# Optimization experiments

Hardware: AMD Instinct MI355X
Metric: run time of the kernel (lower is better)

Reference implementation:

```python
import jax, jax.numpy as jnp
import numpy as np

NEG_SLOPE = 0.2  # PyG GATConv default negative_slope


def _glorot(key, shape):
    fan = shape[0]
    return jax.random.normal(key, shape, dtype=jnp.float32) / np.sqrt(fan)


def setup_inputs() -> dict:
    key = jax.random.key(0)
    ks = jax.random.split(key, 32)
    N, E, C_IN, C_H, C_OUT = 20000, 320000, 128, 640, 2
    inp = {
        "x": jax.random.normal(ks[0], (N, C_IN), dtype=jnp.float32),
        "edge_index": jax.random.randint(ks[1], (2, E), 0, N, dtype=jnp.int64),
    }
    dims = [(C_IN, C_H), (C_H, C_H), (C_H, C_H), (C_H, C_H), (C_H, C_OUT)]
    for i, (ci, co) in enumerate(dims, start=1):
        k = jax.random.split(ks[1 + i], 4)
        inp[f"W{i}"] = _glorot(k[0], (ci, co))
        inp[f"as{i}"] = _glorot(k[1], (co,))
        inp[f"ad{i}"] = _glorot(k[2], (co,))
        inp[f"b{i}"] = jnp.zeros((co,), dtype=jnp.float32)
    return inp


def _gat_conv(h, W, a_src, a_dst, b, src, dst, N):
    # h: [N, Ci] -> hW: [N, Co]
    hW = h @ W
    # per-edge attention logit: LeakyReLU(alpha_src[j] + alpha_dst[i]) for edge j->i
    e = jax.nn.leaky_relu((hW @ a_src)[src] + (hW @ a_dst)[dst], NEG_SLOPE)
    # segment softmax over incoming edges of each dst node (self-loops guarantee nonempty)
    m = jax.ops.segment_max(e, dst, num_segments=N)
    ex = jnp.exp(e - m[dst])
    den = jax.ops.segment_sum(ex, dst, num_segments=N)
    alpha = ex / den[dst]
    # weighted scatter-add of source messages
    out = jax.ops.segment_sum(alpha[:, None] * hW[src], dst, num_segments=N)
    return out + b


def reference(x, edge_index, W1, as1, ad1, b1, W2, as2, ad2, b2, W3, as3, ad3, b3,
              W4, as4, ad4, b4, W5, as5, ad5, b5):
    N = x.shape[0]
    # PyG GATConv default add_self_loops=True
    loops = jnp.arange(N, dtype=edge_index.dtype)
    ei = jnp.concatenate([edge_index, jnp.stack([loops, loops])], axis=1)
    src, dst = ei[0], ei[1]
    h = jax.nn.relu(_gat_conv(x, W1, as1, ad1, b1, src, dst, N))
    h = jax.nn.relu(_gat_conv(h, W2, as2, ad2, b2, src, dst, N))
    h = jax.nn.relu(_gat_conv(h, W3, as3, ad3, b3, src, dst, N))
    h = jax.nn.relu(_gat_conv(h, W4, as4, ad4, b4, src, dst, N))
    # dropout in eval mode = identity
    return _gat_conv(h, W5, as5, ad5, b5, src, dst, N)
```

## Files before the change

kernel.cpp:

```cpp
#include <hip/hip_runtime.h>
#include <math.h>

#define N_NODES 20000
#define MPAD 20096
#define E_EDGES 320000
#define ET (E_EDGES + N_NODES)
#define C_HID 640
#define C_IN 128
#define NEG_SLOPE 0.2f

#define NXB 157
#define NYB 10
#define NXB_FULL 152
#define IDS_MAIN 1520

typedef __attribute__((ext_vector_type(8))) short bf16x8;
typedef __attribute__((ext_vector_type(4))) float f32x4;

__device__ __forceinline__ float leaky(float x) { return x > 0.f ? x : NEG_SLOPE * x; }

__device__ __forceinline__ unsigned short f2bf(float f) {
    unsigned u = __float_as_uint(f);
    unsigned r = (u + 0x7fffu + ((u >> 16) & 1u)) >> 16;
    return (unsigned short)r;
}
__device__ __forceinline__ float bf2f(unsigned short h) {
    return __uint_as_float(((unsigned)h) << 16);
}

__device__ __forceinline__ void gld16(const void* g, void* l) {
    __builtin_amdgcn_global_load_lds((const __attribute__((address_space(1))) unsigned int*)g,
                                     (__attribute__((address_space(3))) unsigned int*)l,
                                     16, 0, 0);
}

__device__ __forceinline__ void decode_xy(int id, int& bx, int& by) {
    if (id < IDS_MAIN) {
        int g = id / 80;
        bx = g * 8 + (id & 7);
        by = (id % 80) >> 3;
    } else {
        int v = id - IDS_MAIN;
        bx = NXB_FULL + v % 5;
        by = v / 5;
    }
}

__global__ void k_zero(int* p, int n) {
    int i = blockIdx.x * blockDim.x + threadIdx.x;
    if (i < n) p[i] = 0;
}

__global__ void k_zerof(float* p, int n) {
    int i = blockIdx.x * blockDim.x + threadIdx.x;
    if (i < n) p[i] = 0.f;
}

__global__ void k_count(const int* __restrict__ ei, int* __restrict__ counts) {
    int j = blockIdx.x * blockDim.x + threadIdx.x;
    if (j >= ET) return;
    int d = (j < E_EDGES) ? ei[E_EDGES + j] : (j - E_EDGES);
    atomicAdd(&counts[d], 1);
}

__global__ __launch_bounds__(1024) void k_scan(int* __restrict__ counts,
                                               int* __restrict__ rowptr) {
    __shared__ int part[1024];
    int t = threadIdx.x;
    int base = t * 20;
    int incl[20];
    int s = 0;
#pragma unroll
    for (int k = 0; k < 20; k++) {
        int i = base + k;
        int v = (i < N_NODES) ? counts[i] : 0;
        s += v;
        incl[k] = s;
    }
    part[t] = s;
    __syncthreads();
    for (int off = 1; off < 1024; off <<= 1) {
        int x = (t >= off) ? part[t - off] : 0;
        __syncthreads();
        part[t] += x;
        __syncthreads();
    }
    int prefix = (t == 0) ? 0 : part[t - 1];
    if (t == 0) rowptr[0] = 0;
#pragma unroll
    for (int k = 0; k < 20; k++) {
        int i = base + k;
        if (i < N_NODES) {
            rowptr[i + 1] = prefix + incl[k];
            counts[i] = (k == 0) ? prefix : prefix + incl[k - 1];
        }
    }
}

__global__ void k_fill(const int* __restrict__ ei, int* __restrict__ cursor, int* __restrict__ col) {
    int j = blockIdx.x * blockDim.x + threadIdx.x;
    if (j >= ET) return;
    int s, d;
    if (j < E_EDGES) { s = ei[j]; d = ei[E_EDGES + j]; }
    else { s = d = j - E_EDGES; }
    int pos = atomicAdd(&cursor[d], 1);
    col[pos] = s;
}

__global__ __launch_bounds__(256) void k_splitWT(const float* __restrict__ W,
                                                 unsigned short* __restrict__ Wth,
                                                 unsigned short* __restrict__ Wtl, int K) {
    __shared__ float tile[64][65];
    int t = threadIdx.x;
    int ki = blockIdx.x * 64, ni = blockIdx.y * 64;
    int tr = t >> 2;
    int tc = (t & 3) * 16;
#pragma unroll
    for (int q = 0; q < 4; ++q) {
        float4 v = *(const float4*)&W[(size_t)(ki + tr) * C_HID + ni + tc + q * 4];
        tile[tr][tc + q * 4 + 0] = v.x;
        tile[tr][tc + q * 4 + 1] = v.y;
        tile[tr][tc + q * 4 + 2] = v.z;
        tile[tr][tc + q * 4 + 3] = v.w;
    }
    __syncthreads();
    unsigned short hh[16], ll[16];
#pragma unroll
    for (int j = 0; j < 16; ++j) {
        float w = tile[tc + j][tr];
        unsigned short h = f2bf(w);
        hh[j] = h;
        ll[j] = f2bf(w - bf2f(h));
    }
    size_t o = (size_t)(ni + tr) * K + ki + tc;
#pragma unroll
    for (int q = 0; q < 4; ++q) {
        *(ushort4*)&Wth[o + q * 4] = make_ushort4(hh[q*4], hh[q*4+1], hh[q*4+2], hh[q*4+3]);
        *(ushort4*)&Wtl[o + q * 4] = make_ushort4(ll[q*4], ll[q*4+1], ll[q*4+2], ll[q*4+3]);
    }
}

__global__ void k_padzero(unsigned short* __restrict__ xah, unsigned short* __restrict__ xal,
                          unsigned short* __restrict__ ph, unsigned short* __restrict__ pl) {
    int idx = blockIdx.x * blockDim.x + threadIdx.x;
    const int nx = (MPAD - N_NODES) * C_IN;
    const int np = (MPAD - N_NODES) * C_HID;
    if (idx < nx) {
        xah[N_NODES * C_IN + idx] = 0;
        xal[N_NODES * C_IN + idx] = 0;
    }
    if (idx < np) {
        ph[N_NODES * C_HID + idx] = 0;
        pl[N_NODES * C_HID + idx] = 0;
    }
}

__global__ void k_wa(const float* __restrict__ W, const float* __restrict__ a_s,
                     const float* __restrict__ a_d,
                     float* __restrict__ ws_, float* __restrict__ wd_) {
    int wave = (blockIdx.x * blockDim.x + threadIdx.x) >> 6;
    int lane = threadIdx.x & 63;
    if (wave >= C_IN) return;
    const float* row = W + (size_t)wave * C_HID;
    float s = 0.f, d = 0.f;
#pragma unroll
    for (int c = lane; c < C_HID; c += 64) {
        float w = row[c];
        s = fmaf(w, a_s[c], s);
        d = fmaf(w, a_d[c], d);
    }
    for (int o = 32; o; o >>= 1) { s += __shfl_xor(s, o); d += __shfl_xor(d, o); }
    if (lane == 0) { ws_[wave] = s; wd_[wave] = d; }
}

__global__ __launch_bounds__(256) void k_logitx(const float* __restrict__ x,
                                                const float* __restrict__ ws_,
                                                const float* __restrict__ wd_,
                                                float* __restrict__ as_, float* __restrict__ ad_) {
    int wave = (blockIdx.x * blockDim.x + threadIdx.x) >> 6;
    int lane = threadIdx.x & 63;
    if (wave >= N_NODES) return;
    float2 xv = ((const float2*)(x + (size_t)wave * C_IN))[lane];
    float2 wsv = ((const float2*)ws_)[lane];
    float2 wdv = ((const float2*)wd_)[lane];
    float s = xv.x * wsv.x + xv.y * wsv.y;
    float d = xv.x * wdv.x + xv.y * wdv.y;
    for (int o = 32; o; o >>= 1) { s += __shfl_xor(s, o); d += __shfl_xor(d, o); }
    if (lane == 0) { as_[wave] = s; ad_[wave] = d; }
}

__global__ __launch_bounds__(256) void k_mfma_gemm(
    const unsigned short* __restrict__ Ahi, const unsigned short* __restrict__ Alo,
    const unsigned short* __restrict__ Bth, const unsigned short* __restrict__ Btl,
    float* __restrict__ C, int K, int M,
    const float* __restrict__ asrc, const float* __restrict__ adst,
    float* __restrict__ as_, float* __restrict__ ad_) {
    __shared__ unsigned short lds[12288];
    const int t = threadIdx.x;
    const int lane = t & 63, wv = t >> 6;
    const int wm = wv >> 1, wn = wv & 1;
    const int quad = lane >> 4, cl = lane & 15;
    int bx, by;
    decode_xy(blockIdx.x, bx, by);
    const int rowBase = bx * 128;
    const int colBase = by * 64;
    const int r4 = t >> 2, c8 = (t & 3) * 8;

    f32x4 acc[4][2];
#pragma unroll
    for (int i = 0; i < 4; i++)
#pragma unroll
        for (int j = 0; j < 2; j++)
            acc[i][j] = (f32x4){0.f, 0.f, 0.f, 0.f};

    for (int k0 = 0; k0 < K; k0 += 32) {
        __syncthreads();
#pragma unroll
        for (int p = 0; p < 2; ++p) {
            int row = p * 64 + r4;
            size_t ga = (size_t)(rowBase + row) * K + k0 + c8;
            int lo = row * 32 + c8;
            gld16(Ahi + ga, &lds[lo]);
            gld16(Alo + ga, &lds[4096 + lo]);
        }
        {
            size_t gb = (size_t)(colBase + r4) * K + k0 + c8;
            int lo = r4 * 32 + c8;
            gld16(Bth + gb, &lds[8192 + lo]);
            gld16(Btl + gb, &lds[10240 + lo]);
        }
        __syncthreads();

        bf16x8 ah[4], al[4], bh[2], bl[2];
#pragma unroll
        for (int i = 0; i < 4; ++i) {
            int am = (wm * 64 + i * 16 + cl) * 32 + quad * 8;
            ah[i] = *(const bf16x8*)&lds[am];
            al[i] = *(const bf16x8*)&lds[4096 + am];
        }
#pragma unroll
        for (int j = 0; j < 2; ++j) {
            int bn = (wn * 32 + j * 16 + cl) * 32 + quad * 8;
            bh[j] = *(const bf16x8*)&lds[8192 + bn];
            bl[j] = *(const bf16x8*)&lds[10240 + bn];
        }
#pragma unroll
        for (int i = 0; i < 4; ++i)
#pragma unroll
            for (int j = 0; j < 2; ++j) {
                acc[i][j] = __builtin_amdgcn_mfma_f32_16x16x32_bf16(ah[i], bh[j], acc[i][j], 0, 0, 0);
                acc[i][j] = __builtin_amdgcn_mfma_f32_16x16x32_bf16(ah[i], bl[j], acc[i][j], 0, 0, 0);
                acc[i][j] = __builtin_amdgcn_mfma_f32_16x16x32_bf16(al[i], bh[j], acc[i][j], 0, 0, 0);
            }
    }

#pragma unroll
    for (int i = 0; i < 4; ++i)
#pragma unroll
        for (int j = 0; j < 2; ++j) {
            int colC = colBase + wn * 32 + j * 16 + cl;
#pragma unroll
            for (int rr = 0; rr < 4; ++rr) {
                int rowC = rowBase + wm * 64 + i * 16 + quad * 4 + rr;
                if (rowC < M) C[(size_t)rowC * C_HID + colC] = acc[i][j][rr];
            }
        }

    float av[2], dv[2];
#pragma unroll
    for (int j = 0; j < 2; ++j) {
        int cn = colBase + wn * 32 + j * 16 + cl;
        av[j] = asrc[cn];
        dv[j] = adst[cn];
    }
#pragma unroll
    for (int i = 0; i < 4; ++i)
#pragma unroll
        for (int rr = 0; rr < 4; ++rr) {
            float s = 0.f, d = 0.f;
#pragma unroll
            for (int j = 0; j < 2; ++j) {
                float v = acc[i][j][rr];
                s = fmaf(v, av[j], s);
                d = fmaf(v, dv[j], d);
            }
#pragma unroll
            for (int o = 8; o >= 1; o >>= 1) {
                s += __shfl_xor(s, o);
                d += __shfl_xor(d, o);
            }
            int rowC = rowBase + wm * 64 + i * 16 + quad * 4 + rr;
            if (cl == 0 && rowC < M) {
                atomicAdd(&as_[rowC], s);
                atomicAdd(&ad_[rowC], d);
            }
        }
}

__global__ __launch_bounds__(256) void k_mfma_gemm_pair(
    const unsigned short* __restrict__ Ahi, const unsigned short* __restrict__ Alo,
    const unsigned short* __restrict__ Bth, const unsigned short* __restrict__ Btl,
    unsigned short* __restrict__ Oh, unsigned short* __restrict__ Ol,
    const float* __restrict__ bias, int K, int M) {
    __shared__ unsigned short lds[12288];
    const int t = threadIdx.x;
    const int lane = t & 63, wv = t >> 6;
    const int wm = wv >> 1, wn = wv & 1;
    const int quad = lane >> 4, cl = lane & 15;
    int bx, by;
    decode_xy(blockIdx.x, bx, by);
    const int rowBase = bx * 128;
    const int colBase = by * 64;
    const int r4 = t >> 2, c8 = (t & 3) * 8;

    f32x4 acc[4][2];
#pragma unroll
    for (int i = 0; i < 4; i++)
#pragma unroll
        for (int j = 0; j < 2; j++)
            acc[i][j] = (f32x4){0.f, 0.f, 0.f, 0.f};

    for (int k0 = 0; k0 < K; k0 += 32) {
        __syncthreads();
#pragma unroll
        for (int p = 0; p < 2; ++p) {
            int row = p * 64 + r4;
            size_t ga = (size_t)(rowBase + row) * K + k0 + c8;
            int lo = row * 32 + c8;
            gld16(Ahi + ga, &lds[lo]);
            gld16(Alo + ga, &lds[4096 + lo]);
        }
        {
            size_t gb = (size_t)(colBase + r4) * K + k0 + c8;
            int lo = r4 * 32 + c8;
            gld16(Bth + gb, &lds[8192 + lo]);
            gld16(Btl + gb, &lds[10240 + lo]);
        }
        __syncthreads();

        bf16x8 ah[4], al[4], bh[2], bl[2];
#pragma unroll
        for (int i = 0; i < 4; ++i) {
            int am = (wm * 64 + i * 16 + cl) * 32 + quad * 8;
            ah[i] = *(const bf16x8*)&lds[am];
            al[i] = *(const bf16x8*)&lds[4096 + am];
        }
#pragma unroll
        for (int j = 0; j < 2; ++j) {
            int bn = (wn * 32 + j * 16 + cl) * 32 + quad * 8;
            bh[j] = *(const bf16x8*)&lds[8192 + bn];
            bl[j] = *(const bf16x8*)&lds[10240 + bn];
        }
#pragma unroll
        for (int i = 0; i < 4; ++i)
#pragma unroll
            for (int j = 0; j < 2; ++j) {
                acc[i][j] = __builtin_amdgcn_mfma_f32_16x16x32_bf16(ah[i], bh[j], acc[i][j], 0, 0, 0);
                acc[i][j] = __builtin_amdgcn_mfma_f32_16x16x32_bf16(ah[i], bl[j], acc[i][j], 0, 0, 0);
                acc[i][j] = __builtin_amdgcn_mfma_f32_16x16x32_bf16(al[i], bh[j], acc[i][j], 0, 0, 0);
            }
    }

#pragma unroll
    for (int j = 0; j < 2; ++j) {
        int colC = colBase + wn * 32 + j * 16 + cl;
        float bv = bias[colC];
#pragma unroll
        for (int i = 0; i < 4; ++i)
#pragma unroll
            for (int rr = 0; rr < 4; ++rr) {
                int rowC = rowBase + wm * 64 + i * 16 + quad * 4 + rr;
                if (rowC < M) {
                    float v = fmaxf(acc[i][j][rr] + bv, 0.f);
                    unsigned short h = f2bf(v);
                    Oh[(size_t)rowC * C_HID + colC] = h;
                    Ol[(size_t)rowC * C_HID + colC] = f2bf(v - bf2f(h));
                }
            }
    }
}

__global__ __launch_bounds__(256) void k_gather(const float* __restrict__ hW,
                                                const float* __restrict__ as_,
                                                const float* __restrict__ ad_,
                                                const int* __restrict__ rowptr,
                                                const int* __restrict__ col,
                                                const float* __restrict__ bias,
                                                unsigned short* __restrict__ outh,
                                                unsigned short* __restrict__ outl) {
    int wv = threadIdx.x >> 6, lane = threadIdx.x & 63;
    int node = blockIdx.x * 4 + wv;
    int c = blockIdx.y;
    if (node >= N_NODES) return;
    int start = rowptr[node], end = rowptr[node + 1];
    int deg = end - start;
    const float* base = hW + c * 128 + lane * 2;
    float ax = 0.f, ay = 0.f;
    float adi = ad_[node];

    if (deg <= 64) {
        int col_v = col[start + min(lane, deg - 1)];
        float asv = as_[col_v];
        float logit = (lane < deg) ? leaky(asv + adi) : -1e30f;
        float m = logit;
#pragma unroll
        for (int o = 32; o; o >>= 1) m = fmaxf(m, __shfl_xor(m, o));
        float ex = __expf(logit - m);
        float den = ex;
#pragma unroll
        for (int o = 32; o; o >>= 1) den += __shfl_xor(den, o);
        float alpha_v = ex / den;

        for (int e0 = 0; e0 < deg; e0 += 8) {
            float2 r[8];
            float a[8];
#pragma unroll
            for (int q = 0; q < 8; ++q) {
                int e = e0 + q;
                int ec = min(e, deg - 1);
                int s = __shfl(col_v, ec);
                float ar = __shfl(alpha_v, ec);
                a[q] = (e < deg) ? ar : 0.f;
                r[q] = *(const float2*)(base + (size_t)s * C_HID);
            }
#pragma unroll
            for (int q = 0; q < 8; ++q) {
                ax = fmaf(a[q], r[q].x, ax);
                ay = fmaf(a[q], r[q].y, ay);
            }
        }
    } else {
        float m = -1e30f;
        for (int j = start + lane; j < end; j += 64)
            m = fmaxf(m, leaky(as_[col[j]] + adi));
        for (int o = 32; o; o >>= 1) m = fmaxf(m, __shfl_xor(m, o));
        float den = 0.f;
        for (int j = start + lane; j < end; j += 64)
            den += __expf(leaky(as_[col[j]] + adi) - m);
        for (int o = 32; o; o >>= 1) den += __shfl_xor(den, o);
        float inv = 1.f / den;
        for (int j = start; j < end; ++j) {
            int s = col[j];
            float a = __expf(leaky(as_[s] + adi) - m) * inv;
            float2 r = *(const float2*)(base + (size_t)s * C_HID);
            ax = fmaf(a, r.x, ax);
            ay = fmaf(a, r.y, ay);
        }
    }

    float2 b = *(const float2*)&bias[c * 128 + lane * 2];
    float v0 = fmaxf(ax + b.x, 0.f);
    float v1 = fmaxf(ay + b.y, 0.f);
    unsigned short h0 = f2bf(v0), h1 = f2bf(v1);
    size_t o = (size_t)node * C_HID + c * 128 + lane * 2;
    *(ushort2*)&outh[o] = make_ushort2(h0, h1);
    *(ushort2*)&outl[o] = make_ushort2(f2bf(v0 - bf2f(h0)), f2bf(v1 - bf2f(h1)));
}

__global__ __launch_bounds__(256) void k_gather_x(const float* __restrict__ x,
                                                  const float* __restrict__ as_,
                                                  const float* __restrict__ ad_,
                                                  const int* __restrict__ rowptr,
                                                  const int* __restrict__ col,
                                                  unsigned short* __restrict__ outh,
                                                  unsigned short* __restrict__ outl) {
    int wv = threadIdx.x >> 6, lane = threadIdx.x & 63;
    int node = blockIdx.x * 4 + wv;
    if (node >= N_NODES) return;
    int start = rowptr[node], end = rowptr[node + 1];
    int deg = end - start;
    const float* base = x + lane * 2;
    float ax = 0.f, ay = 0.f;
    float adi = ad_[node];

    if (deg <= 64) {
        int col_v = col[start + min(lane, deg - 1)];
        float asv = as_[col_v];
        float logit = (lane < deg) ? leaky(asv + adi) : -1e30f;
        float m = logit;
#pragma unroll
        for (int o = 32; o; o >>= 1) m = fmaxf(m, __shfl_xor(m, o));
        float ex = __expf(logit - m);
        float den = ex;
#pragma unroll
        for (int o = 32; o; o >>= 1) den += __shfl_xor(den, o);
        float alpha_v = ex / den;

        for (int e0 = 0; e0 < deg; e0 += 8) {
            float2 r[8];
            float a[8];
#pragma unroll
            for (int q = 0; q < 8; ++q) {
                int e = e0 + q;
                int ec = min(e, deg - 1);
                int s = __shfl(col_v, ec);
                float ar = __shfl(alpha_v, ec);
                a[q] = (e < deg) ? ar : 0.f;
                r[q] = *(const float2*)(base + (size_t)s * C_IN);
            }
#pragma unroll
            for (int q = 0; q < 8; ++q) {
                ax = fmaf(a[q], r[q].x, ax);
                ay = fmaf(a[q], r[q].y, ay);
            }
        }
    } else {
        float m = -1e30f;
        for (int j = start + lane; j < end; j += 64)
            m = fmaxf(m, leaky(as_[col[j]] + adi));
        for (int o = 32; o; o >>= 1) m = fmaxf(m, __shfl_xor(m, o));
        float den = 0.f;
        for (int j = start + lane; j < end; j += 64)
            den += __expf(leaky(as_[col[j]] + adi) - m);
        for (int o = 32; o; o >>= 1) den += __shfl_xor(den, o);
        float inv = 1.f / den;
        for (int j = start; j < end; ++j) {
            int s = col[j];
            float a = __expf(leaky(as_[s] + adi) - m) * inv;
            float2 r = *(const float2*)(base + (size_t)s * C_IN);
            ax = fmaf(a, r.x, ax);
            ay = fmaf(a, r.y, ay);
        }
    }

    unsigned short h0 = f2bf(ax), h1 = f2bf(ay);
    size_t o = (size_t)node * C_IN + lane * 2;
    *(ushort2*)&outh[o] = make_ushort2(h0, h1);
    *(ushort2*)&outl[o] = make_ushort2(f2bf(ax - bf2f(h0)), f2bf(ay - bf2f(h1)));
}

__global__ __launch_bounds__(256) void k_gemm2(const unsigned short* __restrict__ hh,
                                               const unsigned short* __restrict__ hl,
                                               const float* __restrict__ W,
                                               const float* __restrict__ asrc,
                                               const float* __restrict__ adst,
                                               float* __restrict__ hW5,
                                               float* __restrict__ as_,
                                               float* __restrict__ ad_) {
    int wave = (blockIdx.x * blockDim.x + threadIdx.x) >> 6;
    int lane = threadIdx.x & 63;
    if (wave >= N_NODES) return;
    const ushort2* rh = (const ushort2*)(hh + (size_t)wave * C_HID);
    const ushort2* rl = (const ushort2*)(hl + (size_t)wave * C_HID);
    float a0 = 0.f, a1 = 0.f;
#pragma unroll
    for (int k2 = lane; k2 < C_HID / 2; k2 += 64) {
        ushort2 h2 = rh[k2];
        ushort2 l2 = rl[k2];
        float v0 = bf2f(h2.x) + bf2f(l2.x);
        float v1 = bf2f(h2.y) + bf2f(l2.y);
        int k = k2 * 2;
        a0 = fmaf(v0, W[k * 2 + 0], a0);
        a1 = fmaf(v0, W[k * 2 + 1], a1);
        a0 = fmaf(v1, W[k * 2 + 2], a0);
        a1 = fmaf(v1, W[k * 2 + 3], a1);
    }
    for (int o = 32; o; o >>= 1) { a0 += __shfl_xor(a0, o); a1 += __shfl_xor(a1, o); }
    if (lane == 0) {
        hW5[wave * 2 + 0] = a0;
        hW5[wave * 2 + 1] = a1;
        as_[wave] = a0 * asrc[0] + a1 * asrc[1];
        ad_[wave] = a0 * adst[0] + a1 * adst[1];
    }
}

__global__ __launch_bounds__(256) void k_agg2(const float* __restrict__ hW5,
                                              const float* __restrict__ as_,
                                              const float* __restrict__ ad_,
                                              const int* __restrict__ rowptr,
                                              const int* __restrict__ col,
                                              const float* __restrict__ bias,
                                              float* __restrict__ out) {
    int wv = threadIdx.x >> 6, lane = threadIdx.x & 63;
    int node = blockIdx.x * 4 + wv;
    if (node >= N_NODES) return;
    int start = rowptr[node], end = rowptr[node + 1];
    int deg = end - start;
    float adi = ad_[node];
    float o0, o1;
    if (deg <= 64) {
        int cv = col[start + min(lane, deg - 1)];
        float logit = (lane < deg) ? leaky(as_[cv] + adi) : -1e30f;
        float m = logit;
#pragma unroll
        for (int o = 32; o; o >>= 1) m = fmaxf(m, __shfl_xor(m, o));
        float ex = __expf(logit - m);
        float den = ex;
#pragma unroll
        for (int o = 32; o; o >>= 1) den += __shfl_xor(den, o);
        float al = ex / den;
        float2 hv = make_float2(0.f, 0.f);
        if (lane < deg) hv = *(const float2*)&hW5[cv * 2];
        o0 = al * hv.x; o1 = al * hv.y;
#pragma unroll
        for (int o = 32; o; o >>= 1) { o0 += __shfl_xor(o0, o); o1 += __shfl_xor(o1, o); }
    } else {
        float m = -1e30f;
        for (int j = start + lane; j < end; j += 64)
            m = fmaxf(m, leaky(as_[col[j]] + adi));
        for (int o = 32; o; o >>= 1) m = fmaxf(m, __shfl_xor(m, o));
        float den = 0.f;
        for (int j = start + lane; j < end; j += 64)
            den += __expf(leaky(as_[col[j]] + adi) - m);
        for (int o = 32; o; o >>= 1) den += __shfl_xor(den, o);
        float inv = 1.f / den;
        o0 = 0.f; o1 = 0.f;
        for (int j = start + lane; j < end; j += 64) {
            int s = col[j];
            float al = __expf(leaky(as_[s] + adi) - m) * inv;
            o0 = fmaf(al, hW5[s * 2 + 0], o0);
            o1 = fmaf(al, hW5[s * 2 + 1], o1);
        }
        for (int o = 32; o; o >>= 1) { o0 += __shfl_xor(o0, o); o1 += __shfl_xor(o1, o); }
    }
    if (lane == 0) {
        out[node * 2 + 0] = o0 + bias[0];
        out[node * 2 + 1] = o1 + bias[1];
    }
}

extern "C" void kernel_launch(void* const* d_in, const int* in_sizes, int n_in,
                              void* d_out, int out_size, void* d_ws, size_t ws_size,
                              hipStream_t stream) {
    const float* x   = (const float*)d_in[0];
    const int*   ei  = (const int*)d_in[1];
    const float* W[5]  = {(const float*)d_in[2],  (const float*)d_in[6],
                          (const float*)d_in[10], (const float*)d_in[14],
                          (const float*)d_in[18]};
    const float* As[5] = {(const float*)d_in[3],  (const float*)d_in[7],
                          (const float*)d_in[11], (const float*)d_in[15],
                          (const float*)d_in[19]};
    const float* Ad[5] = {(const float*)d_in[4],  (const float*)d_in[8],
                          (const float*)d_in[12], (const float*)d_in[16],
                          (const float*)d_in[20]};
    const float* Bi[5] = {(const float*)d_in[5],  (const float*)d_in[9],
                          (const float*)d_in[13], (const float*)d_in[17],
                          (const float*)d_in[21]};
    float* out = (float*)d_out;

    char* w = (char*)d_ws;
    float* bufX = (float*)w;                 w += (size_t)N_NODES * C_HID * 4;
    unsigned short* xa_hi = (unsigned short*)bufX;
    unsigned short* xa_lo = xa_hi + (size_t)MPAD * C_IN;
    unsigned short* pair_hi = (unsigned short*)w; w += (size_t)MPAD * C_HID * 2;
    unsigned short* pair_lo = (unsigned short*)w; w += (size_t)MPAD * C_HID * 2;
    unsigned short* Wth = (unsigned short*)w;     w += (size_t)C_HID * C_HID * 2;
    unsigned short* Wtl = (unsigned short*)w;     w += (size_t)C_HID * C_HID * 2;
    float* as_  = (float*)w;  w += N_NODES * 4;
    float* ad_  = (float*)w;  w += N_NODES * 4;
    float* hW5  = (float*)w;  w += N_NODES * 2 * 4;
    float* ws_  = (float*)w;  w += C_IN * 4;
    float* wd_  = (float*)w;  w += C_IN * 4;
    int* rowptr = (int*)w;    w += (N_NODES + 1) * 4 + 12;
    int* counts = (int*)w;    w += N_NODES * 4;
    int* col    = (int*)w;    w += ET * 4;

    const int TB = 256;
    k_zero<<<(N_NODES + TB - 1) / TB, TB, 0, stream>>>(counts, N_NODES);
    k_count<<<(ET + TB - 1) / TB, TB, 0, stream>>>(ei, counts);
    k_scan<<<1, 1024, 0, stream>>>(counts, rowptr);
    k_fill<<<(ET + TB - 1) / TB, TB, 0, stream>>>(ei, counts, col);

    k_padzero<<<((MPAD - N_NODES) * C_HID + TB - 1) / TB, TB, 0, stream>>>(xa_hi, xa_lo, pair_hi, pair_lo);

    const int gemmBlocks = NXB * NYB;
    dim3 gathGrid(N_NODES / 4, 5);
    int nodeWaveBlocks = (N_NODES + 3) / 4;

    k_splitWT<<<dim3(C_IN / 64, C_HID / 64), TB, 0, stream>>>(W[0], Wth, Wtl, C_IN);
    k_wa<<<32, TB, 0, stream>>>(W[0], As[0], Ad[0], ws_, wd_);
    k_logitx<<<nodeWaveBlocks, TB, 0, stream>>>(x, ws_, wd_, as_, ad_);
    k_gather_x<<<nodeWaveBlocks, TB, 0, stream>>>(x, as_, ad_, rowptr, col, xa_hi, xa_lo);
    k_mfma_gemm_pair<<<gemmBlocks, TB, 0, stream>>>(xa_hi, xa_lo, Wth, Wtl,
                                                    pair_hi, pair_lo, Bi[0], C_IN, N_NODES);

    for (int l = 1; l <= 3; ++l) {
        k_zerof<<<(2 * N_NODES + TB - 1) / TB, TB, 0, stream>>>(as_, 2 * N_NODES);
        k_splitWT<<<dim3(C_HID / 64, C_HID / 64), TB, 0, stream>>>(W[l], Wth, Wtl, C_HID);
        k_mfma_gemm<<<gemmBlocks, TB, 0, stream>>>(pair_hi, pair_lo, Wth, Wtl, bufX, C_HID, N_NODES,
                                                   As[l], Ad[l], as_, ad_);
        k_gather<<<gathGrid, TB, 0, stream>>>(bufX, as_, ad_, rowptr, col, Bi[l], pair_hi, pair_lo);
    }

    k_gemm2<<<nodeWaveBlocks, TB, 0, stream>>>(pair_hi, pair_lo, W[4], As[4], Ad[4], hW5, as_, ad_);
    k_agg2<<<nodeWaveBlocks, TB, 0, stream>>>(hW5, as_, ad_, rowptr, col, Bi[4], out);
}
```

Baseline: 764.7 us.

## Precompute per-edge attention weights once, narrow gather to 64-column slices

```diff
diff --git a/kernel.cpp b/kernel.cpp
--- a/kernel.cpp
+++ b/kernel.cpp
@@ -187,6 +187,29 @@
     float d = xv.x * wdv.x + xv.y * wdv.y;
     for (int o = 32; o; o >>= 1) { s += __shfl_xor(s, o); d += __shfl_xor(d, o); }
     if (lane == 0) { as_[wave] = s; ad_[wave] = d; }
+}
+
+__global__ __launch_bounds__(256) void k_alpha(const float* __restrict__ as_,
+                                               const float* __restrict__ ad_,
+                                               const int* __restrict__ rowptr,
+                                               const int* __restrict__ col,
+                                               float* __restrict__ alpha) {
+    int wave = (blockIdx.x * blockDim.x + threadIdx.x) >> 6;
+    int lane = threadIdx.x & 63;
+    if (wave >= N_NODES) return;
+    int start = rowptr[wave], end = rowptr[wave + 1];
+    float adi = ad_[wave];
+    float m = -1e30f;
+    for (int j = start + lane; j < end; j += 64)
+        m = fmaxf(m, leaky(as_[col[j]] + adi));
+    for (int o = 32; o; o >>= 1) m = fmaxf(m, __shfl_xor(m, o));
+    float den = 0.f;
+    for (int j = start + lane; j < end; j += 64)
+        den += __expf(leaky(as_[col[j]] + adi) - m);
+    for (int o = 32; o; o >>= 1) den += __shfl_xor(den, o);
+    float inv = 1.f / den;
+    for (int j = start + lane; j < end; j += 64)
+        alpha[j] = __expf(leaky(as_[col[j]] + adi) - m) * inv;
 }
 
 __global__ __launch_bounds__(256) void k_mfma_gemm(
@@ -380,39 +403,28 @@
     }
 }
 
-__global__ __launch_bounds__(256) void k_gather(const float* __restrict__ hW,
-                                                const float* __restrict__ as_,
-                                                const float* __restrict__ ad_,
-                                                const int* __restrict__ rowptr,
-                                                const int* __restrict__ col,
-                                                const float* __restrict__ bias,
-                                                unsigned short* __restrict__ outh,
-                                                unsigned short* __restrict__ outl) {
+__global__ __launch_bounds__(256) void k_gather64(const float* __restrict__ hW,
+                                                  const float* __restrict__ alpha,
+                                                  const int* __restrict__ rowptr,
+                                                  const int* __restrict__ col,
+                                                  const float* __restrict__ bias,
+                                                  unsigned short* __restrict__ outh,
+                                                  unsigned short* __restrict__ outl) {
     int wv = threadIdx.x >> 6, lane = threadIdx.x & 63;
     int node = blockIdx.x * 4 + wv;
     int c = blockIdx.y;
     if (node >= N_NODES) return;
     int start = rowptr[node], end = rowptr[node + 1];
     int deg = end - start;
-    const float* base = hW + c * 128 + lane * 2;
-    float ax = 0.f, ay = 0.f;
-    float adi = ad_[node];
+    const float* base = hW + c * 64 + lane;
+    float ax = 0.f;
 
     if (deg <= 64) {
-        int col_v = col[start + min(lane, deg - 1)];
-        float asv = as_[col_v];
-        float logit = (lane < deg) ? leaky(asv + adi) : -1e30f;
-        float m = logit;
-#pragma unroll
-        for (int o = 32; o; o >>= 1) m = fmaxf(m, __shfl_xor(m, o));
-        float ex = __expf(logit - m);
-        float den = ex;
-#pragma unroll
-        for (int o = 32; o; o >>= 1) den += __shfl_xor(den, o);
-        float alpha_v = ex / den;
-
+        int idx = start + min(lane, deg - 1);
+        int col_v = col[idx];
+        float alpha_v = alpha[idx];
         for (int e0 = 0; e0 < deg; e0 += 8) {
-            float2 r[8];
+            float r[8];
             float a[8];
 #pragma unroll
             for (int q = 0; q < 8; ++q) {
@@ -421,45 +433,29 @@
                 int s = __shfl(col_v, ec);
                 float ar = __shfl(alpha_v, ec);
                 a[q] = (e < deg) ? ar : 0.f;
-                r[q] = *(const float2*)(base + (size_t)s * C_HID);
-            }
-#pragma unroll
-            for (int q = 0; q < 8; ++q) {
-                ax = fmaf(a[q], r[q].x, ax);
-                ay = fmaf(a[q], r[q].y, ay);
-            }
+                r[q] = base[(size_t)s * C_HID];
+            }
+#pragma unroll
+            for (int q = 0; q < 8; ++q)
+                ax = fmaf(a[q], r[q], ax);
         }
     } else {
-        float m = -1e30f;
-        for (int j = start + lane; j < end; j += 64)
-            m = fmaxf(m, leaky(as_[col[j]] + adi));
-        for (int o = 32; o; o >>= 1) m = fmaxf(m, __shfl_xor(m, o));
-        float den = 0.f;
-        for (int j = start + lane; j < end; j += 64)
-            den += __expf(leaky(as_[col[j]] + adi) - m);
-        for (int o = 32; o; o >>= 1) den += __shfl_xor(den, o);
-        float inv = 1.f / den;
         for (int j = start; j < end; ++j) {
             int s = col[j];
-            float a = __expf(leaky(as_[s] + adi) - m) * inv;
-            float2 r = *(const float2*)(base + (size_t)s * C_HID);
-            ax = fmaf(a, r.x, ax);
-            ay = fmaf(a, r.y, ay);
-        }
-    }
-
-    float2 b = *(const float2*)&bias[c * 128 + lane * 2];
-    float v0 = fmaxf(ax + b.x, 0.f);
-    float v1 = fmaxf(ay + b.y, 0.f);
-    unsigned short h0 = f2bf(v0), h1 = f2bf(v1);
-    size_t o = (size_t)node * C_HID + c * 128 + lane * 2;
-    *(ushort2*)&outh[o] = make_ushort2(h0, h1);
-    *(ushort2*)&outl[o] = make_ushort2(f2bf(v0 - bf2f(h0)), f2bf(v1 - bf2f(h1)));
+            float a = alpha[j];
+            ax = fmaf(a, base[(size_t)s * C_HID], ax);
+        }
+    }
+
+    float v0 = fmaxf(ax + bias[c * 64 + lane], 0.f);
+    unsigned short h0 = f2bf(v0);
+    size_t o = (size_t)node * C_HID + c * 64 + lane;
+    outh[o] = h0;
+    outl[o] = f2bf(v0 - bf2f(h0));
 }
 
 __global__ __launch_bounds__(256) void k_gather_x(const float* __restrict__ x,
-                                                  const float* __restrict__ as_,
-                                                  const float* __restrict__ ad_,
+                                                  const float* __restrict__ alpha,
                                                   const int* __restrict__ rowptr,
                                                   const int* __restrict__ col,
                                                   unsigned short* __restrict__ outh,
@@ -471,21 +467,11 @@
     int deg = end - start;
     const float* base = x + lane * 2;
     float ax = 0.f, ay = 0.f;
-    float adi = ad_[node];
 
     if (deg <= 64) {
-        int col_v = col[start + min(lane, deg - 1)];
-        float asv = as_[col_v];
-        float logit = (lane < deg) ? leaky(asv + adi) : -1e30f;
-        float m = logit;
-#pragma unroll
-        for (int o = 32; o; o >>= 1) m = fmaxf(m, __shfl_xor(m, o));
-        float ex = __expf(logit - m);
-        float den = ex;
-#pragma unroll
-        for (int o = 32; o; o >>= 1) den += __shfl_xor(den, o);
-        float alpha_v = ex / den;
-
+        int idx = start + min(lane, deg - 1);
+        int col_v = col[idx];
+        float alpha_v = alpha[idx];
         for (int e0 = 0; e0 < deg; e0 += 8) {
             float2 r[8];
             float a[8];
@@ -505,18 +491,9 @@
             }
         }
     } else {
-        float m = -1e30f;
-        for (int j = start + lane; j < end; j += 64)
-            m = fmaxf(m, leaky(as_[col[j]] + adi));
-        for (int o = 32; o; o >>= 1) m = fmaxf(m, __shfl_xor(m, o));
-        float den = 0.f;
-        for (int j = start + lane; j < end; j += 64)
-            den += __expf(leaky(as_[col[j]] + adi) - m);
-        for (int o = 32; o; o >>= 1) den += __shfl_xor(den, o);
-        float inv = 1.f / den;
         for (int j = start; j < end; ++j) {
             int s = col[j];
-            float a = __expf(leaky(as_[s] + adi) - m) * inv;
+            float a = alpha[j];
             float2 r = *(const float2*)(base + (size_t)s * C_IN);
             ax = fmaf(a, r.x, ax);
             ay = fmaf(a, r.y, ay);
@@ -651,6 +628,7 @@
     float* hW5  = (float*)w;  w += N_NODES * 2 * 4;
     float* ws_  = (float*)w;  w += C_IN * 4;
     float* wd_  = (float*)w;  w += C_IN * 4;
+    float* alpha = (float*)w; w += ET * 4;
     int* rowptr = (int*)w;    w += (N_NODES + 1) * 4 + 12;
     int* counts = (int*)w;    w += N_NODES * 4;
     int* col    = (int*)w;    w += ET * 4;
@@ -664,13 +642,14 @@
     k_padzero<<<((MPAD - N_NODES) * C_HID + TB - 1) / TB, TB, 0, stream>>>(xa_hi, xa_lo, pair_hi, pair_lo);
 
     const int gemmBlocks = NXB * NYB;
-    dim3 gathGrid(N_NODES / 4, 5);
+    dim3 gathGrid(N_NODES / 4, 10);
     int nodeWaveBlocks = (N_NODES + 3) / 4;
 
     k_splitWT<<<dim3(C_IN / 64, C_HID / 64), TB, 0, stream>>>(W[0], Wth, Wtl, C_IN);
     k_wa<<<32, TB, 0, stream>>>(W[0], As[0], Ad[0], ws_, wd_);
     k_logitx<<<nodeWaveBlocks, TB, 0, stream>>>(x, ws_, wd_, as_, ad_);
-    k_gather_x<<<nodeWaveBlocks, TB, 0, stream>>>(x, as_, ad_, rowptr, col, xa_hi, xa_lo);
+    k_alpha<<<nodeWaveBlocks, TB, 0, stream>>>(as_, ad_, rowptr, col, alpha);
+    k_gather_x<<<nodeWaveBlocks, TB, 0, stream>>>(x, alpha, rowptr, col, xa_hi, xa_lo);
     k_mfma_gemm_pair<<<gemmBlocks, TB, 0, stream>>>(xa_hi, xa_lo, Wth, Wtl,
                                                     pair_hi, pair_lo, Bi[0], C_IN, N_NODES);
 
@@ -679,7 +658,8 @@
         k_splitWT<<<dim3(C_HID / 64, C_HID / 64), TB, 0, stream>>>(W[l], Wth, Wtl, C_HID);
         k_mfma_gemm<<<gemmBlocks, TB, 0, stream>>>(pair_hi, pair_lo, Wth, Wtl, bufX, C_HID, N_NODES,
                                                    As[l], Ad[l], as_, ad_);
-        k_gather<<<gathGrid, TB, 0, stream>>>(bufX, as_, ad_, rowptr, col, Bi[l], pair_hi, pair_lo);
+        k_alpha<<<nodeWaveBlocks, TB, 0, stream>>>(as_, ad_, rowptr, col, alpha);
+        k_gather64<<<gathGrid, TB, 0, stream>>>(bufX, alpha, rowptr, col, Bi[l], pair_hi, pair_lo);
     }
 
     k_gemm2<<<nodeWaveBlocks, TB, 0, stream>>>(pair_hi, pair_lo, W[4], As[4], Ad[4], hW5, as_, ad_);
```

Result: slower. 796.7 us (+4.2%).
